# Performance work log

Hardware: AMD Instinct MI355X
Metric: run time of the kernel (lower is better)

## Reference

```python
import jax, jax.numpy as jnp
import numpy as np

N = 4096
H = 512
NUM_HEADS = 8
HEAD_DIM = H // NUM_HEADS
NUM_SETS = 1365


def setup_inputs() -> dict:
    key = jax.random.key(0)
    ks = jax.random.split(key, 24)
    s = 1.0 / np.sqrt(H)
    def lin(i):
        W = jax.random.normal(ks[i], (H, H), dtype=jnp.float32) * s
        b = jnp.zeros((H,), dtype=jnp.float32)
        return W, b
    Ws, bs = lin(0)
    Wq1, bq1 = lin(1); Wk1, bk1 = lin(2); Wv1, bv1 = lin(3); Wo1, bo1 = lin(4)
    Wq2, bq2 = lin(5); Wk2, bk2 = lin(6); Wv2, bv2 = lin(7); Wo2, bo2 = lin(8)
    # beta init is zeros in the module; use small nonzero so attention path matters
    beta1 = jnp.array([0.1], dtype=jnp.float32)
    beta2 = jnp.array([0.1], dtype=jnp.float32)
    embeddings = jax.random.normal(ks[9], (N, H), dtype=jnp.float32)
    batch_indices = jnp.sort(jax.random.randint(ks[10], (N,), 0, NUM_SETS))
    return dict(embeddings=embeddings, batch_indices=batch_indices,
                Ws=Ws, bs=bs,
                Wq1=Wq1, bq1=bq1, Wk1=Wk1, bk1=bk1, Wv1=Wv1, bv1=bv1, Wo1=Wo1, bo1=bo1, beta1=beta1,
                Wq2=Wq2, bq2=bq2, Wk2=Wk2, bk2=bk2, Wv2=Wv2, bv2=bv2, Wo2=Wo2, bo2=bo2, beta2=beta2)


def _attn_layer(x, mask, Wq, bq, Wk, bk, Wv, bv, Wo, bo, beta):
    n = x.shape[0]
    q = (x @ Wq + bq).reshape(n, NUM_HEADS, HEAD_DIM)
    k = (x @ Wk + bk).reshape(n, NUM_HEADS, HEAD_DIM)
    v = (x @ Wv + bv).reshape(n, NUM_HEADS, HEAD_DIM)
    scores = jnp.einsum('nhd,mhd->hnm', q, k) / np.sqrt(HEAD_DIM).astype(np.float32)
    scores = jnp.where(mask[None, :, :], scores, -jnp.inf)
    w = jax.nn.softmax(scores, axis=-1)
    w = jnp.nan_to_num(w, nan=0.0)  # rows with no valid key -> 0 (matches torch nan_to_num)
    out = jnp.einsum('hnm,mhd->nhd', w, v).reshape(n, H)
    return beta * (out @ Wo + bo) + x


def reference(embeddings, batch_indices, Ws, bs,
              Wq1, bq1, Wk1, bk1, Wv1, bv1, Wo1, bo1, beta1,
              Wq2, bq2, Wk2, bk2, Wv2, bv2, Wo2, bo2, beta2):
    n = embeddings.shape[0]
    static_emb = jax.nn.relu(embeddings @ Ws + bs)
    same_set = batch_indices[:, None] == batch_indices[None, :]
    mask = same_set & ~jnp.eye(n, dtype=bool)
    dyn = _attn_layer(embeddings, mask, Wq1, bq1, Wk1, bk1, Wv1, bv1, Wo1, bo1, beta1)
    dyn = _attn_layer(dyn, mask, Wq2, bq2, Wk2, bk2, Wv2, bv2, Wo2, bo2, beta2)
    sq = (dyn - static_emb) ** 2
    seg_sum = jax.ops.segment_sum(sq, batch_indices, num_segments=NUM_SETS)
    cnt = jax.ops.segment_sum(jnp.ones((n,), dtype=sq.dtype), batch_indices, num_segments=NUM_SETS)
    return seg_sum / jnp.maximum(cnt, 1.0)[:, None]
```

## Files before the change

### kernel.cpp

```cpp
#include <hip/hip_runtime.h>
#include <hip/hip_bf16.h>
#include <math.h>
#include <stdint.h>

#define N_NODES   4096
#define HDIM      512
#define NUM_HEADS 8
#define HEAD_DIM  64
#define NUM_SETS  1365
#define KDIM      512

typedef __attribute__((ext_vector_type(8))) short bf16x8;
typedef __attribute__((ext_vector_type(4))) float f32x4;

__device__ inline unsigned short f2bfu(float x) {
    __hip_bfloat16 h = __float2bfloat16(x);
    return __builtin_bit_cast(unsigned short, h);
}
__device__ inline float bfu2f(unsigned short u) {
    unsigned v = (unsigned)u << 16;
    return __builtin_bit_cast(float, v);
}

__device__ inline void gload_lds16(const void* g, void* l) {
    __builtin_amdgcn_global_load_lds(
        (const __attribute__((address_space(1))) unsigned int*)g,
        (__attribute__((address_space(3))) unsigned int*)l,
        16, 0, 0);
}

__global__ __launch_bounds__(256) void prep_kernel(
        const float* W0, const float* W1, const float* W2, const float* W3,
        const float* W4, const float* W5, const float* W6, const float* W7,
        const float* W8, __hip_bfloat16* __restrict__ wt,
        const float* __restrict__ emb, __hip_bfloat16* __restrict__ embb,
        const int* __restrict__ batch,
        int* __restrict__ seg_s, int* __restrict__ seg_e) {
    const int bx = blockIdx.x;
    if (bx < 2304) {
        __shared__ float t[32][36];
        const int z = bx >> 8;
        const int tb = bx & 255;
        const float* W = z==0?W0:z==1?W1:z==2?W2:z==3?W3:z==4?W4:z==5?W5:z==6?W6:z==7?W7:W8;
        __hip_bfloat16* Wt = wt + (size_t)z * (512 * 512);
        const int bn = (tb & 15) * 32, bk = (tb >> 4) * 32;
        const int nx = threadIdx.x & 7, ky = threadIdx.x >> 3;
        *(float4*)&t[ky][nx * 4] = *(const float4*)&W[(size_t)(bk + ky) * 512 + bn + nx * 4];
        __syncthreads();
        const int r2 = threadIdx.x >> 3;
        const int ck = threadIdx.x & 7;
        uint2 p;
        p.x = (unsigned)f2bfu(t[ck * 4 + 0][r2]) | ((unsigned)f2bfu(t[ck * 4 + 1][r2]) << 16);
        p.y = (unsigned)f2bfu(t[ck * 4 + 2][r2]) | ((unsigned)f2bfu(t[ck * 4 + 3][r2]) << 16);
        *(uint2*)&Wt[(size_t)(bn + r2) * 512 + bk + ck * 4] = p;
    } else if (bx < 4352) {
        const int i = (bx - 2304) * 256 + threadIdx.x;
        float4 v = ((const float4*)emb)[i];
        uint2 p;
        p.x = (unsigned)f2bfu(v.x) | ((unsigned)f2bfu(v.y) << 16);
        p.y = (unsigned)f2bfu(v.z) | ((unsigned)f2bfu(v.w) << 16);
        ((uint2*)embb)[i] = p;
    } else {
        const int i = (bx - 4352) * 256 + threadIdx.x;
        const int bi = batch[i];
        if (i == 0 || batch[i - 1] != bi) {
            int e = i + 1;
            while (e < N_NODES && batch[e] == bi) ++e;
            for (int j = i; j < e; ++j) { seg_s[j] = i; seg_e[j] = e; }
        }
    }
}

template<int MODE>
__global__ __launch_bounds__(512) void gemm128(
        const __hip_bfloat16* __restrict__ A,
        const __hip_bfloat16* __restrict__ Wt0, const __hip_bfloat16* __restrict__ Wt1,
        const __hip_bfloat16* __restrict__ Wt2, const __hip_bfloat16* __restrict__ Wt3,
        const float* __restrict__ bias0, const float* __restrict__ bias1,
        const float* __restrict__ bias2, const float* __restrict__ bias3,
        __hip_bfloat16* __restrict__ statB, __hip_bfloat16* __restrict__ outB) {
    __shared__ alignas(16) short Al[2][128][64];
    __shared__ alignas(16) short Bl[2][128][64];

    const int tid = threadIdx.x;
    const int wid = tid >> 6, lane = tid & 63;
    const int brow = blockIdx.x * 128;
    const int wsel = blockIdx.y >> 2;
    const int bcol = (blockIdx.y & 3) * 128;
    const __hip_bfloat16* Wt = (wsel == 0) ? Wt0 : (wsel == 1) ? Wt1 : (wsel == 2) ? Wt2 : Wt3;
    const float* bias        = (wsel == 0) ? bias0 : (wsel == 1) ? bias1 : (wsel == 2) ? bias2 : bias3;

    const int swzc = (lane & 7) ^ ((lane >> 3) & 7);
    const __hip_bfloat16* aSrc = A  + (size_t)(brow + wid * 16 + (lane >> 3)) * KDIM + swzc * 8;
    const __hip_bfloat16* bSrc = Wt + (size_t)(bcol + wid * 16 + (lane >> 3)) * KDIM + swzc * 8;

    const int fr = lane & 15, fq = lane >> 4;
    const int rx = fr & 7;
    const int wm = (wid >> 1) * 32;
    const int wn = (wid & 1) * 64;

    auto STAGE = [&](int buf, int t) {
        const int k0 = t * 64;
        gload_lds16(aSrc + k0, &Al[buf][wid * 16][0]);
        gload_lds16(aSrc + k0 + (size_t)8 * KDIM, &Al[buf][wid * 16 + 8][0]);
        gload_lds16(bSrc + k0, &Bl[buf][wid * 16][0]);
        gload_lds16(bSrc + k0 + (size_t)8 * KDIM, &Bl[buf][wid * 16 + 8][0]);
    };

    STAGE(0, 0);
    STAGE(1, 1);

    const int ch0 = ((0 + fq) ^ rx) * 8;
    const int ch1 = ((4 + fq) ^ rx) * 8;

    f32x4 acc[2][4] = {};
    #pragma unroll
    for (int t = 0; t < 8; ++t) {
        const int cur = t & 1;
        if (t < 7) asm volatile("s_waitcnt vmcnt(4)" ::: "memory");
        else       asm volatile("s_waitcnt vmcnt(0)" ::: "memory");
        __builtin_amdgcn_s_barrier();
        __builtin_amdgcn_sched_barrier(0);
        bf16x8 a0[2], a1[2], b0[4], b1[4];
        #pragma unroll
        for (int mi = 0; mi < 2; ++mi) {
            a0[mi] = *(const bf16x8*)&Al[cur][wm + mi * 16 + fr][ch0];
            a1[mi] = *(const bf16x8*)&Al[cur][wm + mi * 16 + fr][ch1];
        }
        #pragma unroll
        for (int ni = 0; ni < 4; ++ni) {
            b0[ni] = *(const bf16x8*)&Bl[cur][wn + ni * 16 + fr][ch0];
            b1[ni] = *(const bf16x8*)&Bl[cur][wn + ni * 16 + fr][ch1];
        }
        __builtin_amdgcn_s_setprio(1);
        #pragma unroll
        for (int mi = 0; mi < 2; ++mi)
            #pragma unroll
            for (int ni = 0; ni < 4; ++ni) {
                acc[mi][ni] = __builtin_amdgcn_mfma_f32_16x16x32_bf16(a0[mi], b0[ni], acc[mi][ni], 0, 0, 0);
                acc[mi][ni] = __builtin_amdgcn_mfma_f32_16x16x32_bf16(a1[mi], b1[ni], acc[mi][ni], 0, 0, 0);
            }
        __builtin_amdgcn_s_setprio(0);
        __builtin_amdgcn_sched_barrier(0);
        __builtin_amdgcn_s_barrier();
        if (t + 2 < 8) STAGE(cur, t + 2);
    }

    float bv[4];
    #pragma unroll
    for (int ni = 0; ni < 4; ++ni) bv[ni] = bias[bcol + wn + ni * 16 + fr];

    #pragma unroll
    for (int mi = 0; mi < 2; ++mi) {
        #pragma unroll
        for (int ni = 0; ni < 4; ++ni) {
            const int c = bcol + wn + ni * 16 + fr;
            #pragma unroll
            for (int r = 0; r < 4; ++r) {
                const int row = brow + wm + mi * 16 + fq * 4 + r;
                const float v = acc[mi][ni][r] + bv[ni];
                if (MODE == 0) {
                    if (wsel == 0) statB[(size_t)row * 512 + c] = __float2bfloat16(fmaxf(v, 0.f));
                    else           outB[(size_t)row * 1536 + (wsel - 1) * 512 + c] = __float2bfloat16(v);
                } else {
                    outB[(size_t)row * 1536 + wsel * 512 + c] = __float2bfloat16(v);
                }
            }
        }
    }
}

__global__ __launch_bounds__(256) void gemm_oproj(
        const __hip_bfloat16* __restrict__ A, const __hip_bfloat16* __restrict__ Wt,
        const float* __restrict__ bias,
        const __hip_bfloat16* __restrict__ X, const float* __restrict__ betaP,
        __hip_bfloat16* __restrict__ outB) {
    __shared__ alignas(16) short Al[2][64][64];
    __shared__ alignas(16) short Bl[2][64][64];

    const int tid = threadIdx.x;
    const int wid = tid >> 6, lane = tid & 63;
    const int brow = blockIdx.x * 64;
    const int bcol = blockIdx.y * 64;

    const int swzc = (lane & 7) ^ ((lane >> 3) & 7);
    const __hip_bfloat16* aSrc = A  + (size_t)(brow + wid * 16 + (lane >> 3)) * KDIM + swzc * 8;
    const __hip_bfloat16* bSrc = Wt + (size_t)(bcol + wid * 16 + (lane >> 3)) * KDIM + swzc * 8;

    const int fr = lane & 15, fq = lane >> 4;
    const int rx = fr & 7;
    const int wm = (wid >> 1) * 32, wn = (wid & 1) * 32;

    auto STAGE = [&](int buf, int t) {
        const int k0 = t * 64;
        gload_lds16(aSrc + k0, &Al[buf][wid * 16][0]);
        gload_lds16(aSrc + k0 + (size_t)8 * KDIM, &Al[buf][wid * 16 + 8][0]);
        gload_lds16(bSrc + k0, &Bl[buf][wid * 16][0]);
        gload_lds16(bSrc + k0 + (size_t)8 * KDIM, &Bl[buf][wid * 16 + 8][0]);
    };

    STAGE(0, 0);
    STAGE(1, 1);

    const int ch0 = ((0 + fq) ^ rx) * 8;
    const int ch1 = ((4 + fq) ^ rx) * 8;

    f32x4 acc[2][2] = {};
    #pragma unroll
    for (int t = 0; t < 8; ++t) {
        const int cur = t & 1;
        if (t < 7) asm volatile("s_waitcnt vmcnt(4)" ::: "memory");
        else       asm volatile("s_waitcnt vmcnt(0)" ::: "memory");
        __builtin_amdgcn_s_barrier();
        __builtin_amdgcn_sched_barrier(0);
        bf16x8 a0[2], a1[2], b0[2], b1[2];
        #pragma unroll
        for (int mi = 0; mi < 2; ++mi) {
            a0[mi] = *(const bf16x8*)&Al[cur][wm + mi * 16 + fr][ch0];
            a1[mi] = *(const bf16x8*)&Al[cur][wm + mi * 16 + fr][ch1];
        }
        #pragma unroll
        for (int ni = 0; ni < 2; ++ni) {
            b0[ni] = *(const bf16x8*)&Bl[cur][wn + ni * 16 + fr][ch0];
            b1[ni] = *(const bf16x8*)&Bl[cur][wn + ni * 16 + fr][ch1];
        }
        __builtin_amdgcn_s_setprio(1);
        #pragma unroll
        for (int mi = 0; mi < 2; ++mi)
            #pragma unroll
            for (int ni = 0; ni < 2; ++ni) {
                acc[mi][ni] = __builtin_amdgcn_mfma_f32_16x16x32_bf16(a0[mi], b0[ni], acc[mi][ni], 0, 0, 0);
                acc[mi][ni] = __builtin_amdgcn_mfma_f32_16x16x32_bf16(a1[mi], b1[ni], acc[mi][ni], 0, 0, 0);
            }
        __builtin_amdgcn_s_setprio(0);
        __builtin_amdgcn_sched_barrier(0);
        __builtin_amdgcn_s_barrier();
        if (t + 2 < 8) STAGE(cur, t + 2);
    }

    float bv[2];
    #pragma unroll
    for (int ni = 0; ni < 2; ++ni) bv[ni] = bias[bcol + wn + ni * 16 + fr];
    const float beta = betaP[0];

    #pragma unroll
    for (int mi = 0; mi < 2; ++mi) {
        #pragma unroll
        for (int ni = 0; ni < 2; ++ni) {
            const int c = bcol + wn + ni * 16 + fr;
            #pragma unroll
            for (int r = 0; r < 4; ++r) {
                const int row = brow + wm + mi * 16 + fq * 4 + r;
                const float xv = __bfloat162float(X[(size_t)row * 512 + c]);
                outB[(size_t)row * 512 + c] =
                    __float2bfloat16(beta * (acc[mi][ni][r] + bv[ni]) + xv);
            }
        }
    }
}

__global__ __launch_bounds__(256) void attn_kernel(
        const __hip_bfloat16* __restrict__ qkv,
        const int* __restrict__ seg_s, const int* __restrict__ seg_e,
        __hip_bfloat16* __restrict__ ab) {
    const int node = (blockIdx.x * blockDim.x + threadIdx.x) >> 6;
    const int lane = threadIdx.x & 63;
    const int c8   = lane * 8;

    bf16x8 q8 = *(const bf16x8*)&qkv[(size_t)node * 1536 + c8];
    float qf[8];
    #pragma unroll
    for (int j = 0; j < 8; ++j) qf[j] = bfu2f((unsigned short)q8[j]);

    const int s = seg_s[node], e = seg_e[node];

    float M = -INFINITY, S = 0.f;
    float o[8] = {};
    for (int m = s; m < e; ++m) {
        if (m == node) continue;
        bf16x8 k8 = *(const bf16x8*)&qkv[(size_t)m * 1536 + 512 + c8];
        float p = 0.f;
        #pragma unroll
        for (int j = 0; j < 8; ++j) p = fmaf(qf[j], bfu2f((unsigned short)k8[j]), p);
        p += __shfl_xor(p, 1, 64);
        p += __shfl_xor(p, 2, 64);
        p += __shfl_xor(p, 4, 64);
        const float sc = p * 0.125f;
        const float newM = fmaxf(M, sc);
        const float scale = __expf(M - newM);
        const float w = __expf(sc - newM);
        S = S * scale + w;
        bf16x8 v8 = *(const bf16x8*)&qkv[(size_t)m * 1536 + 1024 + c8];
        #pragma unroll
        for (int j = 0; j < 8; ++j) o[j] = fmaf(w, bfu2f((unsigned short)v8[j]), o[j] * scale);
        M = newM;
    }
    const float inv = (S > 0.f) ? (1.f / S) : 0.f;
    bf16x8 r;
    #pragma unroll
    for (int j = 0; j < 8; ++j) r[j] = (short)f2bfu(o[j] * inv);
    *(bf16x8*)&ab[(size_t)node * 512 + c8] = r;
}

__global__ __launch_bounds__(256) void seg_mse_kernel(
        const unsigned short* __restrict__ dyn, const unsigned short* __restrict__ stat,
        const int* __restrict__ batch, float* __restrict__ out) {
    const int s = blockIdx.x;
    const int d = threadIdx.x * 2;
    int lo = 0, hi = N_NODES;
    while (lo < hi) { int m = (lo + hi) >> 1; if (batch[m] < s) lo = m + 1; else hi = m; }
    const int a = lo;
    hi = N_NODES;
    while (lo < hi) { int m = (lo + hi) >> 1; if (batch[m] <= s) lo = m + 1; else hi = m; }
    const int b = lo;

    float acc0 = 0.f, acc1 = 0.f;
    for (int i = a; i < b; ++i) {
        const unsigned dv = *(const unsigned*)&dyn[(size_t)i * 512 + d];
        const unsigned sv = *(const unsigned*)&stat[(size_t)i * 512 + d];
        const float d0 = bfu2f((unsigned short)(dv & 0xffff)) - bfu2f((unsigned short)(sv & 0xffff));
        const float d1 = bfu2f((unsigned short)(dv >> 16))   - bfu2f((unsigned short)(sv >> 16));
        acc0 += d0 * d0; acc1 += d1 * d1;
    }
    const float inv = 1.f / fmaxf((float)(b - a), 1.f);
    float2 r; r.x = acc0 * inv; r.y = acc1 * inv;
    *(float2*)&out[(size_t)s * 512 + d] = r;
}

extern "C" void kernel_launch(void* const* d_in, const int* in_sizes, int n_in,
                              void* d_out, int out_size, void* d_ws, size_t ws_size,
                              hipStream_t stream) {
    const float* emb   = (const float*)d_in[0];
    const int*   batch = (const int*)  d_in[1];
    const float* Ws_   = (const float*)d_in[2];
    const float* bs_   = (const float*)d_in[3];
    const float* Wq1 = (const float*)d_in[4];  const float* bq1 = (const float*)d_in[5];
    const float* Wk1 = (const float*)d_in[6];  const float* bk1 = (const float*)d_in[7];
    const float* Wv1 = (const float*)d_in[8];  const float* bv1 = (const float*)d_in[9];
    const float* Wo1 = (const float*)d_in[10]; const float* bo1 = (const float*)d_in[11];
    const float* beta1 = (const float*)d_in[12];
    const float* Wq2 = (const float*)d_in[13]; const float* bq2 = (const float*)d_in[14];
    const float* Wk2 = (const float*)d_in[15]; const float* bk2 = (const float*)d_in[16];
    const float* Wv2 = (const float*)d_in[17]; const float* bv2 = (const float*)d_in[18];
    const float* Wo2 = (const float*)d_in[19]; const float* bo2 = (const float*)d_in[20];
    const float* beta2 = (const float*)d_in[21];

    char* w = (char*)d_ws;
    const size_t MB = 1024 * 1024;
    __hip_bfloat16* statB  = (__hip_bfloat16*)(w + 0 * MB);
    __hip_bfloat16* qkv    = (__hip_bfloat16*)(w + 4 * MB);
    __hip_bfloat16* embb   = (__hip_bfloat16*)(w + 16 * MB);
    __hip_bfloat16* ab     = (__hip_bfloat16*)(w + 20 * MB);
    __hip_bfloat16* dynb   = (__hip_bfloat16*)(w + 24 * MB);
    __hip_bfloat16* dyn2b  = (__hip_bfloat16*)(w + 28 * MB);
    __hip_bfloat16* wt     = (__hip_bfloat16*)(w + 32 * MB);
    int* seg_s = (int*)(w + 37 * MB);
    int* seg_e = seg_s + N_NODES;

    const size_t WSZ = 512 * 512;
    __hip_bfloat16* wtS  = wt + 0 * WSZ;
    __hip_bfloat16* wtQ1 = wt + 1 * WSZ;
    __hip_bfloat16* wtK1 = wt + 2 * WSZ;
    __hip_bfloat16* wtV1 = wt + 3 * WSZ;
    __hip_bfloat16* wtO1 = wt + 4 * WSZ;
    __hip_bfloat16* wtQ2 = wt + 5 * WSZ;
    __hip_bfloat16* wtK2 = wt + 6 * WSZ;
    __hip_bfloat16* wtV2 = wt + 7 * WSZ;
    __hip_bfloat16* wtO2 = wt + 8 * WSZ;

    prep_kernel<<<4368, 256, 0, stream>>>(
        Ws_, Wq1, Wk1, Wv1, Wo1, Wq2, Wk2, Wv2, Wo2, wt,
        emb, embb, batch, seg_s, seg_e);

    gemm128<0><<<dim3(32, 16), 512, 0, stream>>>(
        embb, wtS, wtQ1, wtK1, wtV1, bs_, bq1, bk1, bv1, statB, qkv);
    attn_kernel<<<N_NODES / 4, 256, 0, stream>>>(qkv, seg_s, seg_e, ab);
    gemm_oproj<<<dim3(64, 8), 256, 0, stream>>>(ab, wtO1, bo1, embb, beta1, dynb);

    gemm128<1><<<dim3(32, 12), 512, 0, stream>>>(
        dynb, wtQ2, wtK2, wtV2, wtV2, bq2, bk2, bv2, bv2, nullptr, qkv);
    attn_kernel<<<N_NODES / 4, 256, 0, stream>>>(qkv, seg_s, seg_e, ab);
    gemm_oproj<<<dim3(64, 8), 256, 0, stream>>>(ab, wtO2, bo2, dynb, beta2, dyn2b);

    seg_mse_kernel<<<NUM_SETS, 256, 0, stream>>>(
        (const unsigned short*)dyn2b, (const unsigned short*)statB, batch, (float*)d_out);
}
```

Measured before the change: 75.54 us.

## Fuse segment MSE into final o-proj GEMM and remap blocks across XCDs

Removes the separate seg_mse kernel and the dyn2 buffer write/read: the final o-projection epilogue now computes the squared difference against the static embedding, scales it by the inverse set size, and atomically adds it into the zeroed output. Both GEMM kernels also remap the linear block id so that consecutive blocks landing on the same XCD share row tiles, which is meant to improve L2 reuse. The change adds a memset, many fp32 atomics on small segments, and nondeterministic summation order.

Result: slower. 82.09 us (+8.7%).

```diff
diff --git a/kernel.cpp b/kernel.cpp
--- a/kernel.cpp
+++ b/kernel.cpp
@@ -84,9 +84,15 @@
 
     const int tid = threadIdx.x;
     const int wid = tid >> 6, lane = tid & 63;
-    const int brow = blockIdx.x * 128;
-    const int wsel = blockIdx.y >> 2;
-    const int bcol = (blockIdx.y & 3) * 128;
+    constexpr int NY = (MODE == 0) ? 16 : 12;
+    const int hwid = blockIdx.y * gridDim.x + blockIdx.x;
+    const int xcd = hwid & 7;
+    const int t8  = hwid >> 3;
+    const int bg  = t8 / NY;
+    const int yy  = t8 % NY;
+    const int brow = (bg * 8 + xcd) * 128;
+    const int wsel = yy >> 2;
+    const int bcol = (yy & 3) * 128;
     const __hip_bfloat16* Wt = (wsel == 0) ? Wt0 : (wsel == 1) ? Wt1 : (wsel == 2) ? Wt2 : Wt3;
     const float* bias        = (wsel == 0) ? bias0 : (wsel == 1) ? bias1 : (wsel == 2) ? bias2 : bias3;
 
@@ -170,18 +176,26 @@
     }
 }
 
+template<bool MSE>
 __global__ __launch_bounds__(256) void gemm_oproj(
         const __hip_bfloat16* __restrict__ A, const __hip_bfloat16* __restrict__ Wt,
         const float* __restrict__ bias,
         const __hip_bfloat16* __restrict__ X, const float* __restrict__ betaP,
-        __hip_bfloat16* __restrict__ outB) {
+        __hip_bfloat16* __restrict__ outB,
+        const unsigned short* __restrict__ statB,
+        const int* __restrict__ batch,
+        const int* __restrict__ seg_s, const int* __restrict__ seg_e,
+        float* __restrict__ outMse) {
     __shared__ alignas(16) short Al[2][64][64];
     __shared__ alignas(16) short Bl[2][64][64];
 
     const int tid = threadIdx.x;
     const int wid = tid >> 6, lane = tid & 63;
-    const int brow = blockIdx.x * 64;
-    const int bcol = blockIdx.y * 64;
+    const int hwid = blockIdx.y * gridDim.x + blockIdx.x;
+    const int xcd = hwid & 7;
+    const int t8  = hwid >> 3;
+    const int brow = ((t8 >> 3) * 8 + xcd) * 64;
+    const int bcol = (t8 & 7) * 64;
 
     const int swzc = (lane & 7) ^ ((lane >> 3) & 7);
     const __hip_bfloat16* aSrc = A  + (size_t)(brow + wid * 16 + (lane >> 3)) * KDIM + swzc * 8;
@@ -243,6 +257,19 @@
     for (int ni = 0; ni < 2; ++ni) bv[ni] = bias[bcol + wn + ni * 16 + fr];
     const float beta = betaP[0];
 
+    int   rbi[2][4];
+    float rinv[2][4];
+    if (MSE) {
+        #pragma unroll
+        for (int mi = 0; mi < 2; ++mi)
+            #pragma unroll
+            for (int r = 0; r < 4; ++r) {
+                const int row = brow + wm + mi * 16 + fq * 4 + r;
+                rbi[mi][r]  = batch[row];
+                rinv[mi][r] = 1.f / fmaxf((float)(seg_e[row] - seg_s[row]), 1.f);
+            }
+    }
+
     #pragma unroll
     for (int mi = 0; mi < 2; ++mi) {
         #pragma unroll
@@ -252,8 +279,13 @@
             for (int r = 0; r < 4; ++r) {
                 const int row = brow + wm + mi * 16 + fq * 4 + r;
                 const float xv = __bfloat162float(X[(size_t)row * 512 + c]);
-                outB[(size_t)row * 512 + c] =
-                    __float2bfloat16(beta * (acc[mi][ni][r] + bv[ni]) + xv);
+                const float v = beta * (acc[mi][ni][r] + bv[ni]) + xv;
+                if (!MSE) {
+                    outB[(size_t)row * 512 + c] = __float2bfloat16(v);
+                } else {
+                    const float sd = v - bfu2f(statB[(size_t)row * 512 + c]);
+                    atomicAdd(&outMse[(size_t)rbi[mi][r] * 512 + c], sd * sd * rinv[mi][r]);
+                }
             }
         }
     }
@@ -300,31 +332,6 @@
     #pragma unroll
     for (int j = 0; j < 8; ++j) r[j] = (short)f2bfu(o[j] * inv);
     *(bf16x8*)&ab[(size_t)node * 512 + c8] = r;
-}
-
-__global__ __launch_bounds__(256) void seg_mse_kernel(
-        const unsigned short* __restrict__ dyn, const unsigned short* __restrict__ stat,
-        const int* __restrict__ batch, float* __restrict__ out) {
-    const int s = blockIdx.x;
-    const int d = threadIdx.x * 2;
-    int lo = 0, hi = N_NODES;
-    while (lo < hi) { int m = (lo + hi) >> 1; if (batch[m] < s) lo = m + 1; else hi = m; }
-    const int a = lo;
-    hi = N_NODES;
-    while (lo < hi) { int m = (lo + hi) >> 1; if (batch[m] <= s) lo = m + 1; else hi = m; }
-    const int b = lo;
-
-    float acc0 = 0.f, acc1 = 0.f;
-    for (int i = a; i < b; ++i) {
-        const unsigned dv = *(const unsigned*)&dyn[(size_t)i * 512 + d];
-        const unsigned sv = *(const unsigned*)&stat[(size_t)i * 512 + d];
-        const float d0 = bfu2f((unsigned short)(dv & 0xffff)) - bfu2f((unsigned short)(sv & 0xffff));
-        const float d1 = bfu2f((unsigned short)(dv >> 16))   - bfu2f((unsigned short)(sv >> 16));
-        acc0 += d0 * d0; acc1 += d1 * d1;
-    }
-    const float inv = 1.f / fmaxf((float)(b - a), 1.f);
-    float2 r; r.x = acc0 * inv; r.y = acc1 * inv;
-    *(float2*)&out[(size_t)s * 512 + d] = r;
 }
 
 extern "C" void kernel_launch(void* const* d_in, const int* in_sizes, int n_in,
@@ -352,9 +359,8 @@
     __hip_bfloat16* embb   = (__hip_bfloat16*)(w + 16 * MB);
     __hip_bfloat16* ab     = (__hip_bfloat16*)(w + 20 * MB);
     __hip_bfloat16* dynb   = (__hip_bfloat16*)(w + 24 * MB);
-    __hip_bfloat16* dyn2b  = (__hip_bfloat16*)(w + 28 * MB);
-    __hip_bfloat16* wt     = (__hip_bfloat16*)(w + 32 * MB);
-    int* seg_s = (int*)(w + 37 * MB);
+    __hip_bfloat16* wt     = (__hip_bfloat16*)(w + 28 * MB);
+    int* seg_s = (int*)(w + 33 * MB);
     int* seg_e = seg_s + N_NODES;
 
     const size_t WSZ = 512 * 512;
@@ -368,6 +374,8 @@
     __hip_bfloat16* wtV2 = wt + 7 * WSZ;
     __hip_bfloat16* wtO2 = wt + 8 * WSZ;
 
+    hipMemsetAsync(d_out, 0, (size_t)out_size * sizeof(float), stream);
+
     prep_kernel<<<4368, 256, 0, stream>>>(
         Ws_, Wq1, Wk1, Wv1, Wo1, Wq2, Wk2, Wv2, Wo2, wt,
         emb, embb, batch, seg_s, seg_e);
@@ -375,13 +383,13 @@
     gemm128<0><<<dim3(32, 16), 512, 0, stream>>>(
         embb, wtS, wtQ1, wtK1, wtV1, bs_, bq1, bk1, bv1, statB, qkv);
     attn_kernel<<<N_NODES / 4, 256, 0, stream>>>(qkv, seg_s, seg_e, ab);
-    gemm_oproj<<<dim3(64, 8), 256, 0, stream>>>(ab, wtO1, bo1, embb, beta1, dynb);
+    gemm_oproj<false><<<dim3(64, 8), 256, 0, stream>>>(
+        ab, wtO1, bo1, embb, beta1, dynb, nullptr, nullptr, nullptr, nullptr, nullptr);
 
     gemm128<1><<<dim3(32, 12), 512, 0, stream>>>(
         dynb, wtQ2, wtK2, wtV2, wtV2, bq2, bk2, bv2, bv2, nullptr, qkv);
     attn_kernel<<<N_NODES / 4, 256, 0, stream>>>(qkv, seg_s, seg_e, ab);
-    gemm_oproj<<<dim3(64, 8), 256, 0, stream>>>(ab, wtO2, bo2, dynb, beta2, dyn2b);
-
-    seg_mse_kernel<<<NUM_SETS, 256, 0, stream>>>(
-        (const unsigned short*)dyn2b, (const unsigned short*)statB, batch, (float*)d_out);
-}
+    gemm_oproj<true><<<dim3(64, 8), 256, 0, stream>>>(
+        ab, wtO2, bo2, dynb, beta2, nullptr,
+        (const unsigned short*)statB, batch, seg_s, seg_e, (float*)d_out);
+}
```
